# Kernel tuning notes

Hardware: AMD Instinct MI355X
Metric: run time of the kernel (lower is better)

Reference implementation:

```python
import jax, jax.numpy as jnp
import numpy as np

B, S, H, L, C = 32, 512, 768, 512, 3  # batch, seq, hidden, max_length, num_classes


def _lin_init(k, fan_in, shape):
    return jax.random.normal(k, shape, jnp.float32) * (1.0 / np.sqrt(fan_in))


def setup_inputs() -> dict:
    key = jax.random.key(0)
    ks = jax.random.split(key, 18)
    return {
        "tokens": jax.random.normal(ks[0], (B, S, H), jnp.float32),
        # shared Q/K/V projections (used for both token- and feature-attention)
        "Wq": _lin_init(ks[1], H, (H, H)), "bq": jnp.zeros((H,), jnp.float32),
        "Wk": _lin_init(ks[2], H, (H, H)), "bk": jnp.zeros((H,), jnp.float32),
        "Wv": _lin_init(ks[3], H, (H, H)), "bv": jnp.zeros((H,), jnp.float32),
        # TSGSA: Linear(H,1)+ReLU gate over tokens
        "W_ts": _lin_init(ks[4], H, (H, 1)), "b_ts": jnp.zeros((1,), jnp.float32),
        # FSGSA: Linear(max_length,1)+ReLU gate over padded seq axis (also reused for FGSA per source bug)
        "W_fs": _lin_init(ks[5], L, (L, 1)), "b_fs": jnp.zeros((1,), jnp.float32),
        # TGSA: Linear(H,H)+Sigmoid gate
        "W_tg": _lin_init(ks[6], H, (H, H)), "b_tg": jnp.zeros((H,), jnp.float32),
        # fnn: Linear(7H,H) -> Linear(H,C)
        "W1": _lin_init(ks[7], 7 * H, (7 * H, H)), "b1": jnp.zeros((H,), jnp.float32),
        "W2": _lin_init(ks[8], H, (H, C)), "b2": jnp.zeros((C,), jnp.float32),
    }


def _ln(x):
    # LayerNorm over (seq, hidden) jointly, eps=1e-8; freshly-instantiated affine params are identity
    m = jnp.mean(x, axis=(1, 2), keepdims=True)
    v = jnp.var(x, axis=(1, 2), keepdims=True)
    return (x - m) * jax.lax.rsqrt(v + 1e-8)


def reference(tokens, Wq, bq, Wk, bk, Wv, bv, W_ts, b_ts, W_fs, b_fs, W_tg, b_tg, W1, b1, W2, b2):
    scale = 1.0 / np.sqrt(H)
    Q = tokens @ Wq + bq  # [B,S,H]
    K = tokens @ Wk + bk
    V = tokens @ Wv + bv
    # token-direction self-attention: softmax(Q K^T / sqrt(H)) V
    att = jax.nn.softmax(jnp.einsum('bsh,bth->bst', Q, K) * scale, axis=-1)  # [B,S,S]
    TSA = jnp.einsum('bst,bth->bsh', att, V)
    # feature-direction self-attention: V @ softmax(Q^T K / sqrt(H))
    attN = jax.nn.softmax(jnp.einsum('bsh,bsg->bhg', Q, K) * scale, axis=-1)  # [B,H,H]
    FSA = jnp.einsum('bsh,bhg->bsg', V, attN)
    # gate branches
    TSGSA = jax.nn.relu(tokens @ W_ts + b_ts) * tokens  # [B,S,1]*[B,S,H]
    tpad = jnp.pad(tokens.transpose(0, 2, 1), ((0, 0), (0, 0), (0, L - S)))  # [B,H,L]
    gate_f = jax.nn.relu(tpad @ W_fs + b_fs)  # [B,H,1]
    FSGSA = (gate_f * tokens.transpose(0, 2, 1)).transpose(0, 2, 1)  # [B,S,H]
    TGSA = jax.nn.sigmoid(tokens @ W_tg + b_tg) * tokens
    FGSA = FSGSA  # source bug: FGSA branch applies self.FSGSA, identical to FSGSA
    out_all = jnp.concatenate(
        [tokens, _ln(TSA), _ln(FSA), _ln(TGSA), _ln(FGSA), _ln(TSGSA), _ln(FSGSA)], axis=2)  # [B,S,7H]
    pooled = jnp.mean(out_all, axis=1)  # [B,7H]
    return (pooled @ W1 + b1) @ W2 + b2  # [B,C]
```

## Files before the change

kernel.cpp:

```cpp
#include <hip/hip_runtime.h>
#include <cmath>

typedef unsigned short u16;
typedef __attribute__((ext_vector_type(4))) float f32x4;
typedef __attribute__((ext_vector_type(4))) unsigned int u32x4;
typedef __attribute__((ext_vector_type(8))) __bf16 bf16x8;

__device__ __forceinline__ u16 f2b(float f) {
  unsigned int u = __builtin_bit_cast(unsigned int, f);
  return (u16)((u + 0x7fffu + ((u >> 16) & 1u)) >> 16);
}
__device__ __forceinline__ float b2f(u16 h) {
  unsigned int u = ((unsigned int)h) << 16;
  return __builtin_bit_cast(float, u);
}

__device__ __forceinline__ void glds16(const u16* g, u16* l) {
  __builtin_amdgcn_global_load_lds(
      (const __attribute__((address_space(1))) void*)g,
      (__attribute__((address_space(3))) void*)l, 16, 0, 0);
}

template <int EPI>
__global__ __launch_bounds__(256) void gemm_f_k(
    const u16* __restrict__ Ap, const u16* __restrict__ Bp, u16* __restrict__ Cp,
    u16* __restrict__ CpT, const float* __restrict__ bias,
    const float* __restrict__ tokp, float* __restrict__ colsum,
    float* __restrict__ bstat, int K, int lda, int ldb, int ldc, long sA,
    long sB, long sC, float scale) {
  __shared__ alignas(16) u16 smem[4][4096];

  const int gx = gridDim.x, gxy = gx * gridDim.y;
  const int nwg = gxy * gridDim.z;
  int orig = (blockIdx.z * gridDim.y + blockIdx.y) * gx + blockIdx.x;
  int gwi = (orig & 7) * (nwg >> 3) + (orig >> 3);
  const int z = gwi / gxy;
  int rem = gwi - z * gxy;
  const int ty = rem / gx, tx = rem - ty * gx;
  const int tileM = ty << 7, tileN = tx << 7;

  const u16* Abase = Ap + (size_t)z * sA;
  const u16* Bbase = Bp + (size_t)z * sB;

  const int tid = threadIdx.x;
  const int lane = tid & 63, w = tid >> 6;
  const int wr = (w >> 1) << 6, wc = (w & 1) << 6;
  const int fr = lane & 15, fg = lane >> 4;

  f32x4 acc[4][4];
#pragma unroll
  for (int i = 0; i < 4; ++i)
#pragma unroll
    for (int j = 0; j < 4; ++j) acc[i][j] = (f32x4){0.f, 0.f, 0.f, 0.f};

  const int srow = (w << 5) + (lane >> 2);
  const int scol = (((lane & 3) ^ ((lane >> 3) & 3)) << 3);
  const u16* gA = Abase + (size_t)(tileM + srow) * lda + scol;
  const u16* gB = Bbase + (size_t)(tileN + srow) * ldb + scol;
  const int ldsw = (w << 5) * 32;

  auto STAGE = [&](int buf, int k0) {
    const u16* ga = gA + k0;
    const u16* gb = gB + k0;
    u16* la = &smem[buf * 2][ldsw];
    u16* lb = &smem[buf * 2 + 1][ldsw];
    glds16(ga, la);
    glds16(ga + (size_t)16 * lda, la + 512);
    glds16(gb, lb);
    glds16(gb + (size_t)16 * ldb, lb + 512);
  };

  const int col_off = ((fg ^ ((fr >> 1) & 3)) << 3);

  const int nt = K >> 5;
  STAGE(0, 0);
  int cur = 0;
  for (int t = 0; t < nt; ++t) {
    if (t + 1 < nt) {
      STAGE(cur ^ 1, (t + 1) << 5);
      asm volatile("s_waitcnt vmcnt(4)" ::: "memory");
    } else {
      asm volatile("s_waitcnt vmcnt(0)" ::: "memory");
    }
    __builtin_amdgcn_s_barrier();
    asm volatile("" ::: "memory");
    const u16* Ab = smem[cur * 2];
    const u16* Bb = smem[cur * 2 + 1];
    bf16x8 av[4], bw[4];
#pragma unroll
    for (int m = 0; m < 4; ++m)
      av[m] = *(const bf16x8*)&Ab[(wr + (m << 4) + fr) * 32 + col_off];
#pragma unroll
    for (int n = 0; n < 4; ++n)
      bw[n] = *(const bf16x8*)&Bb[(wc + (n << 4) + fr) * 32 + col_off];
#pragma unroll
    for (int m = 0; m < 4; ++m)
#pragma unroll
      for (int n = 0; n < 4; ++n)
        acc[m][n] =
            __builtin_amdgcn_mfma_f32_16x16x32_bf16(av[m], bw[n], acc[m][n], 0, 0, 0);
    asm volatile("" ::: "memory");
    __builtin_amdgcn_s_barrier();
    cur ^= 1;
  }

  if constexpr (EPI == 0 || EPI == 2) {
    int cbuf = 0, nbase = tileN;
    if constexpr (EPI == 0) { cbuf = tileN / 768; nbase = tileN - cbuf * 768; }
    u16* Cz = Cp + (EPI == 0 ? (size_t)cbuf * sC : (size_t)z * sC);
#pragma unroll
    for (int m = 0; m < 4; ++m) {
#pragma unroll
      for (int n = 0; n < 4; ++n) {
        const int gcol = tileN + wc + (n << 4) + fr;
        const int lcol = nbase + wc + (n << 4) + fr;
#pragma unroll
        for (int r = 0; r < 4; ++r) {
          const int grow = tileM + wr + (m << 4) + (fg << 2) + r;
          float v = acc[m][n][r];
          if constexpr (EPI == 0) v += bias[gcol];
          else v *= scale;
          Cz[(size_t)grow * ldc + lcol] = f2b(v);
        }
      }
    }
    if constexpr (EPI == 0) {
      u16* Ct = CpT + (size_t)cbuf * sC;
#pragma unroll
      for (int m = 0; m < 4; ++m) {
#pragma unroll
        for (int n = 0; n < 4; ++n) {
          const int gcol = tileN + wc + (n << 4) + fr;
          const int lcol = nbase + wc + (n << 4) + fr;
          const int grow0 = tileM + wr + (m << 4) + (fg << 2);
          union { u16 u[4]; unsigned long long q; } pk;
#pragma unroll
          for (int r = 0; r < 4; ++r) pk.u[r] = f2b(acc[m][n][r] + bias[gcol]);
          *(unsigned long long*)&Ct[(size_t)lcol * 16384 + grow0] = pk.q;
        }
      }
    }
  } else {
    __shared__ float scol_s[128];
    __shared__ float sred[2];
    if (tid < 128) scol_s[tid] = 0.f;
    if (tid == 0) { sred[0] = 0.f; sred[1] = 0.f; }
    __syncthreads();
    float ls = 0.f, lq = 0.f;
#pragma unroll
    for (int n = 0; n < 4; ++n) {
      float cpart = 0.f;
      const int gcol = tileN + wc + (n << 4) + fr;
#pragma unroll
      for (int m = 0; m < 4; ++m) {
#pragma unroll
        for (int r = 0; r < 4; ++r) {
          float v = acc[m][n][r];
          if constexpr (EPI == 1) {
            const int grow = tileM + wr + (m << 4) + (fg << 2) + r;
            float pre = v + bias[gcol];
            float g = 1.f / (1.f + __expf(-pre));
            v = g * tokp[(size_t)grow * 768 + gcol];
          }
          cpart += v; ls += v; lq += v * v;
        }
      }
      atomicAdd(&scol_s[wc + (n << 4) + fr], cpart);
    }
    atomicAdd(&sred[0], ls);
    atomicAdd(&sred[1], lq);
    __syncthreads();
    const int b = (EPI == 1) ? (tileM >> 9) : z;
    if (tid < 128) atomicAdd(&colsum[(size_t)b * 768 + tileN + tid], scol_s[tid]);
    if (tid == 0) {
      atomicAdd(&bstat[b], sred[0]);
      atomicAdd(&bstat[32 + b], sred[1]);
    }
  }
}

__global__ __launch_bounds__(256) void cvt_tok_k(const float* __restrict__ in,
                                                 u16* __restrict__ out) {
  const size_t i = ((size_t)blockIdx.x * 256 + threadIdx.x) * 8;
  f32x4 a = *(const f32x4*)(in + i), b = *(const f32x4*)(in + i + 4);
  union { u16 u[8]; u32x4 q; } pk;
#pragma unroll
  for (int j = 0; j < 4; ++j) { pk.u[j] = f2b(a[j]); pk.u[4 + j] = f2b(b[j]); }
  *(u32x4*)(out + i) = pk.q;
}

__global__ __launch_bounds__(256) void transpose_w_k(const float* __restrict__ W,
                                                     u16* __restrict__ WT) {
  __shared__ float t[64][65];
  const int r0 = blockIdx.y << 6, c0 = blockIdx.x << 6;
  for (int i = threadIdx.x; i < 4096; i += 256) {
    int r = i >> 6, c = i & 63;
    t[r][c] = W[(size_t)(r0 + r) * 768 + c0 + c];
  }
  __syncthreads();
  for (int i = threadIdx.x; i < 4096; i += 256) {
    int rr = i >> 6, cc = i & 63;
    WT[(size_t)(c0 + rr) * 768 + r0 + cc] = f2b(t[cc][rr]);
  }
}

__global__ __launch_bounds__(256) void transpose_bf_k(const u16* __restrict__ in,
                                                      u16* __restrict__ out) {
  __shared__ u16 t[64][72];
  const size_t base = (size_t)blockIdx.z * 589824;
  const int r0 = blockIdx.y << 6, c0 = blockIdx.x << 6;
  for (int i = threadIdx.x; i < 512; i += 256) {
    int r = i >> 3, c8 = (i & 7) << 3;
    union { u32x4 q; u16 u[8]; } pk;
    pk.q = *(const u32x4*)&in[base + (size_t)(r0 + r) * 768 + c0 + c8];
#pragma unroll
    for (int j = 0; j < 8; ++j) t[c8 + j][r] = pk.u[j];
  }
  __syncthreads();
  for (int i = threadIdx.x; i < 512; i += 256) {
    int r = i >> 3, c8 = (i & 7) << 3;
    *(u32x4*)&out[base + (size_t)(c0 + r) * 768 + r0 + c8] = *(u32x4*)&t[r][c8];
  }
}

template <int LEN>
__global__ __launch_bounds__(256) void softmax_k(u16* __restrict__ data) {
  constexpr int NP = LEN / 256;
  const int row = blockIdx.x, tid = threadIdx.x;
  u16* p = data + (size_t)row * LEN;
  const int lane = tid & 63, wid = tid >> 6;
  float v[NP];
  float mx = -1e30f;
#pragma unroll
  for (int i = 0; i < NP; ++i) { v[i] = b2f(p[tid + (i << 8)]); mx = fmaxf(mx, v[i]); }
#pragma unroll
  for (int o = 32; o > 0; o >>= 1) mx = fmaxf(mx, __shfl_xor(mx, o));
  __shared__ float red[4], red2[4];
  if (lane == 0) red[wid] = mx;
  __syncthreads();
  mx = fmaxf(fmaxf(red[0], red[1]), fmaxf(red[2], red[3]));
  float sum = 0.f;
#pragma unroll
  for (int i = 0; i < NP; ++i) { v[i] = __expf(v[i] - mx); sum += v[i]; }
#pragma unroll
  for (int o = 32; o > 0; o >>= 1) sum += __shfl_xor(sum, o);
  if (lane == 0) red2[wid] = sum;
  __syncthreads();
  sum = red2[0] + red2[1] + red2[2] + red2[3];
  const float inv = 1.f / sum;
#pragma unroll
  for (int i = 0; i < NP; ++i) p[tid + (i << 8)] = f2b(v[i] * inv);
}

__global__ __launch_bounds__(256) void row_stats_k(
    const float* __restrict__ tok, const float* __restrict__ Wts,
    const float* __restrict__ bts, float* __restrict__ gate_t,
    float* __restrict__ rowsum, float* __restrict__ rowsumsq) {
  const int wid = threadIdx.x >> 6, lane = threadIdx.x & 63;
  const int row = blockIdx.x * 4 + wid;
  const float* p = tok + (size_t)row * 768;
  float s = 0.f, q = 0.f, g = 0.f;
#pragma unroll
  for (int i = 0; i < 12; ++i) {
    float t = p[lane + i * 64];
    s += t; q += t * t; g += t * Wts[lane + i * 64];
  }
#pragma unroll
  for (int o = 32; o > 0; o >>= 1) {
    s += __shfl_xor(s, o); q += __shfl_xor(q, o); g += __shfl_xor(g, o);
  }
  if (lane == 0) {
    gate_t[row] = fmaxf(g + bts[0], 0.f);
    rowsum[row] = s;
    rowsumsq[row] = q;
  }
}

__global__ __launch_bounds__(256) void col_stats_k(
    const float* __restrict__ tok, const float* __restrict__ Wfs,
    const float* __restrict__ bfs, const float* __restrict__ gate_t,
    float* __restrict__ gate_f, float* __restrict__ colsum_tok,
    float* __restrict__ colsumsq_tok, float* __restrict__ colsum_tsg) {
  const int b = blockIdx.x, h = blockIdx.y * 256 + threadIdx.x;
  const float* p = tok + (size_t)b * 512 * 768 + h;
  const float* gt = gate_t + b * 512;
  float cs = 0.f, cq = 0.f, gf = 0.f, tg = 0.f;
#pragma unroll 4
  for (int s = 0; s < 512; ++s) {
    float t = p[(size_t)s * 768];
    cs += t; cq += t * t; gf += t * Wfs[s]; tg += t * gt[s];
  }
  const int idx = b * 768 + h;
  gate_f[idx] = fmaxf(gf + bfs[0], 0.f);
  colsum_tok[idx] = cs;
  colsumsq_tok[idx] = cq;
  colsum_tsg[idx] = tg;
}

__global__ __launch_bounds__(256) void batch_stats_k(
    const float* __restrict__ gate_t, const float* __restrict__ rowsum,
    const float* __restrict__ rowsumsq, const float* __restrict__ gate_f,
    const float* __restrict__ colsum_tok, const float* __restrict__ colsumsq_tok,
    float* __restrict__ st) {
  __shared__ float red[4][256];
  const int b = blockIdx.x, tid = threadIdx.x;
  float ts = 0.f, tq = 0.f, fs = 0.f, fq = 0.f;
  for (int s = tid; s < 512; s += 256) {
    float g = gate_t[b * 512 + s];
    ts += g * rowsum[b * 512 + s];
    tq += g * g * rowsumsq[b * 512 + s];
  }
  for (int h = tid; h < 768; h += 256) {
    float g = gate_f[b * 768 + h];
    fs += g * colsum_tok[b * 768 + h];
    fq += g * g * colsumsq_tok[b * 768 + h];
  }
  red[0][tid] = ts; red[1][tid] = tq; red[2][tid] = fs; red[3][tid] = fq;
  __syncthreads();
  for (int o = 128; o > 0; o >>= 1) {
    if (tid < o) {
      red[0][tid] += red[0][tid + o];
      red[1][tid] += red[1][tid + o];
      red[2][tid] += red[2][tid + o];
      red[3][tid] += red[3][tid + o];
    }
    __syncthreads();
  }
  if (tid == 0) {
    st[b] = red[0][0]; st[32 + b] = red[1][0];
    st[64 + b] = red[2][0]; st[96 + b] = red[3][0];
  }
}

__global__ __launch_bounds__(768) void pooled_k(
    const float* __restrict__ colsum_tok, const float* __restrict__ colsum_tsa,
    const float* __restrict__ bstat_tsa, const float* __restrict__ colsum_fsa,
    const float* __restrict__ bstat_fsa, const float* __restrict__ colsum_tgsa,
    const float* __restrict__ bstat_tgsa, const float* __restrict__ colsum_tsg,
    const float* __restrict__ gate_f, const float* __restrict__ st,
    float* __restrict__ pooled) {
  const int b = blockIdx.x, h = threadIdx.x;
  const float invS = 1.f / 512.f, invN = 1.f / (512.f * 768.f);
  const int i = b * 768 + h;
  float* pr = pooled + (size_t)b * 5376;
  pr[h] = colsum_tok[i] * invS;
  auto lnslot = [&](int slot, float cs, float bs, float bq) {
    float m = bs * invN;
    float var = bq * invN - m * m;
    pr[slot * 768 + h] = (cs * invS - m) * rsqrtf(var + 1e-8f);
  };
  lnslot(1, colsum_tsa[i], bstat_tsa[b], bstat_tsa[32 + b]);
  lnslot(2, colsum_fsa[i], bstat_fsa[b], bstat_fsa[32 + b]);
  lnslot(3, colsum_tgsa[i], bstat_tgsa[b], bstat_tgsa[32 + b]);
  const float fsg_cs = gate_f[i] * colsum_tok[i];
  lnslot(4, fsg_cs, st[64 + b], st[96 + b]);
  lnslot(5, colsum_tsg[i], st[b], st[32 + b]);
  lnslot(6, fsg_cs, st[64 + b], st[96 + b]);
}

__global__ __launch_bounds__(256) void fnn1_k(const float* __restrict__ pooled,
                                              const float* __restrict__ W1,
                                              float* __restrict__ tmp1) {
  __shared__ float sp[128][36];
  const int c0 = blockIdx.x << 7, k0 = blockIdx.y << 7;
  const int tid = threadIdx.x;
  for (int i = tid; i < 4096; i += 256) {
    int b = i >> 7, j = i & 127;
    sp[j][b] = pooled[(size_t)b * 5376 + k0 + j];
  }
  __syncthreads();
  const int c = c0 + (tid & 127);
  const int u = (tid >> 7) << 4;
  float acc[16];
#pragma unroll
  for (int t = 0; t < 16; ++t) acc[t] = 0.f;
#pragma unroll 4
  for (int j = 0; j < 128; ++j) {
    float w = W1[(size_t)(k0 + j) * 768 + c];
    const f32x4* row = (const f32x4*)&sp[j][u];
#pragma unroll
    for (int t4 = 0; t4 < 4; ++t4) {
      f32x4 v = row[t4];
#pragma unroll
      for (int r = 0; r < 4; ++r) acc[t4 * 4 + r] += v[r] * w;
    }
  }
#pragma unroll
  for (int t = 0; t < 16; ++t) atomicAdd(&tmp1[(u + t) * 768 + c], acc[t]);
}

__global__ __launch_bounds__(256) void fnn2_k(const float* __restrict__ tmp1,
                                              const float* __restrict__ b1,
                                              const float* __restrict__ W2,
                                              const float* __restrict__ b2,
                                              float* __restrict__ out) {
  const int gw = blockIdx.x * 4 + (threadIdx.x >> 6);
  const int lane = threadIdx.x & 63;
  const int b = gw / 3, c = gw % 3;
  float a = 0.f;
#pragma unroll
  for (int i = 0; i < 12; ++i) {
    int k = lane + i * 64;
    a += (tmp1[b * 768 + k] + b1[k]) * W2[k * 3 + c];
  }
#pragma unroll
  for (int o = 32; o > 0; o >>= 1) a += __shfl_xor(a, o);
  if (lane == 0) out[b * 3 + c] = a + b2[c];
}

extern "C" void kernel_launch(void* const* d_in, const int* in_sizes, int n_in,
                              void* d_out, int out_size, void* d_ws, size_t ws_size,
                              hipStream_t stream) {
  const float* tokens = (const float*)d_in[0];
  const float* Wq = (const float*)d_in[1];
  const float* bq = (const float*)d_in[2];
  const float* Wk = (const float*)d_in[3];
  const float* bk = (const float*)d_in[4];
  const float* Wv = (const float*)d_in[5];
  const float* bv = (const float*)d_in[6];
  const float* Wts = (const float*)d_in[7];
  const float* bts = (const float*)d_in[8];
  const float* Wfs = (const float*)d_in[9];
  const float* bfs = (const float*)d_in[10];
  const float* Wtg = (const float*)d_in[11];
  const float* btg = (const float*)d_in[12];
  const float* W1 = (const float*)d_in[13];
  const float* b1 = (const float*)d_in[14];
  const float* W2 = (const float*)d_in[15];
  const float* b2 = (const float*)d_in[16];
  float* out = (float*)d_out;

  char* ws = (char*)d_ws;
  size_t off = 0;
  auto take = [&](size_t bytes) -> char* {
    char* p = ws + off;
    off += (bytes + 255) & ~(size_t)255;
    return p;
  };
  u16* tokb = (u16*)take((size_t)16384 * 768 * 2);
  u16* WqT = (u16*)take((size_t)768 * 768 * 2);
  u16* WkT = (u16*)take((size_t)768 * 768 * 2);
  u16* WvT = (u16*)take((size_t)768 * 768 * 2);
  u16* WtgT = (u16*)take((size_t)768 * 768 * 2);
  u16* Qb = (u16*)take((size_t)16384 * 768 * 2);
  u16* Kb = (u16*)take((size_t)16384 * 768 * 2);
  u16* Vb = (u16*)take((size_t)16384 * 768 * 2);
  u16* Qt = (u16*)take((size_t)768 * 16384 * 2);
  u16* Kt = (u16*)take((size_t)768 * 16384 * 2);
  u16* Vt = (u16*)take((size_t)768 * 16384 * 2);
  u16* attb = (u16*)take((size_t)32 * 512 * 512 * 2);
  u16* attNb = (u16*)take((size_t)32 * 768 * 768 * 2);
  u16* attNt = Qt;
  float* bias3 = (float*)take(2304 * 4);
  char* zbase = ws + off;
  float* colsum_tsa = (float*)take(24576 * 4);
  float* colsum_fsa = (float*)take(24576 * 4);
  float* colsum_tgsa = (float*)take(24576 * 4);
  float* bstat_tsa = (float*)take(64 * 4);
  float* bstat_fsa = (float*)take(64 * 4);
  float* bstat_tgsa = (float*)take(64 * 4);
  float* tmp1 = (float*)take((size_t)32 * 768 * 4);
  size_t zbytes = (size_t)((ws + off) - zbase);
  float* colsum_tsg = (float*)take(24576 * 4);
  float* gate_t = (float*)take(16384 * 4);
  float* rowsum = (float*)take(16384 * 4);
  float* rowsumsq = (float*)take(16384 * 4);
  float* gate_f = (float*)take(24576 * 4);
  float* colsum_tok = (float*)take(24576 * 4);
  float* colsumsq_tok = (float*)take(24576 * 4);
  float* st4 = (float*)take(128 * 4);
  float* pooled = (float*)take((size_t)32 * 5376 * 4);

  hipMemsetAsync(zbase, 0, zbytes, stream);
  hipMemcpyAsync(bias3, bq, 768 * 4, hipMemcpyDeviceToDevice, stream);
  hipMemcpyAsync(bias3 + 768, bk, 768 * 4, hipMemcpyDeviceToDevice, stream);
  hipMemcpyAsync(bias3 + 1536, bv, 768 * 4, hipMemcpyDeviceToDevice, stream);

  const float scale = 1.0f / sqrtf(768.0f);
  const dim3 blk(256);

  cvt_tok_k<<<6144, blk, 0, stream>>>(tokens, tokb);
  transpose_w_k<<<dim3(12, 12), blk, 0, stream>>>(Wq, WqT);
  transpose_w_k<<<dim3(12, 12), blk, 0, stream>>>(Wk, WkT);
  transpose_w_k<<<dim3(12, 12), blk, 0, stream>>>(Wv, WvT);
  transpose_w_k<<<dim3(12, 12), blk, 0, stream>>>(Wtg, WtgT);

  gemm_f_k<0><<<dim3(18, 128, 1), blk, 0, stream>>>(
      tokb, WqT, Qb, Qt, bias3, nullptr, nullptr, nullptr, 768, 768, 768, 768,
      0, 0, 12582912, 0.f);
  gemm_f_k<1><<<dim3(6, 128, 1), blk, 0, stream>>>(
      tokb, WtgT, nullptr, nullptr, btg, tokens, colsum_tgsa, bstat_tgsa, 768,
      768, 768, 0, 0, 0, 0, 0.f);

  gemm_f_k<2><<<dim3(6, 6, 32), blk, 0, stream>>>(
      Qt, Kt, attNb, nullptr, nullptr, nullptr, nullptr, nullptr, 512, 16384,
      16384, 768, 512, 512, 589824, scale);
  softmax_k<768><<<24576, 256, 0, stream>>>(attNb);
  transpose_bf_k<<<dim3(12, 12, 32), blk, 0, stream>>>(attNb, attNt);

  gemm_f_k<2><<<dim3(4, 4, 32), blk, 0, stream>>>(
      Qb, Kb, attb, nullptr, nullptr, nullptr, nullptr, nullptr, 768, 768, 768,
      512, 393216, 393216, 262144, scale);
  softmax_k<512><<<16384, 256, 0, stream>>>(attb);

  gemm_f_k<3><<<dim3(6, 4, 32), blk, 0, stream>>>(
      attb, Vt, nullptr, nullptr, nullptr, nullptr, colsum_tsa, bstat_tsa, 512,
      512, 16384, 0, 262144, 512, 0, 0.f);
  gemm_f_k<3><<<dim3(6, 4, 32), blk, 0, stream>>>(
      Vb, attNt, nullptr, nullptr, nullptr, nullptr, colsum_fsa, bstat_fsa, 768,
      768, 768, 0, 393216, 589824, 0, 0.f);

  row_stats_k<<<4096, blk, 0, stream>>>(tokens, Wts, bts, gate_t, rowsum, rowsumsq);
  col_stats_k<<<dim3(32, 3), blk, 0, stream>>>(tokens, Wfs, bfs, gate_t, gate_f,
                                               colsum_tok, colsumsq_tok, colsum_tsg);
  batch_stats_k<<<32, blk, 0, stream>>>(gate_t, rowsum, rowsumsq, gate_f,
                                        colsum_tok, colsumsq_tok, st4);

  pooled_k<<<32, 768, 0, stream>>>(colsum_tok, colsum_tsa, bstat_tsa, colsum_fsa,
                                   bstat_fsa, colsum_tgsa, bstat_tgsa, colsum_tsg,
                                   gate_f, st4, pooled);
  fnn1_k<<<dim3(6, 42), blk, 0, stream>>>(pooled, W1, tmp1);
  fnn2_k<<<24, blk, 0, stream>>>(tmp1, b1, W2, b2, out);
}
```

Measured before the change: 464.3 us.

## Fuse gate GEMM into QKV GEMM, compute attN transposed, stage transposes in LDS

```diff
diff --git a/kernel.cpp b/kernel.cpp
--- a/kernel.cpp
+++ b/kernel.cpp
@@ -25,10 +25,12 @@
 __global__ __launch_bounds__(256) void gemm_f_k(
     const u16* __restrict__ Ap, const u16* __restrict__ Bp, u16* __restrict__ Cp,
     u16* __restrict__ CpT, const float* __restrict__ bias,
-    const float* __restrict__ tokp, float* __restrict__ colsum,
+    const u16* __restrict__ tokp, float* __restrict__ colsum,
     float* __restrict__ bstat, int K, int lda, int ldb, int ldc, long sA,
     long sB, long sC, float scale) {
   __shared__ alignas(16) u16 smem[4][4096];
+  __shared__ float scol_s[128];
+  __shared__ float sred[2];
 
   const int gx = gridDim.x, gxy = gx * gridDim.y;
   const int nwg = gxy * gridDim.z;
@@ -104,45 +106,100 @@
     cur ^= 1;
   }
 
-  if constexpr (EPI == 0 || EPI == 2) {
-    int cbuf = 0, nbase = tileN;
-    if constexpr (EPI == 0) { cbuf = tileN / 768; nbase = tileN - cbuf * 768; }
-    u16* Cz = Cp + (EPI == 0 ? (size_t)cbuf * sC : (size_t)z * sC);
-#pragma unroll
-    for (int m = 0; m < 4; ++m) {
-#pragma unroll
-      for (int n = 0; n < 4; ++n) {
-        const int gcol = tileN + wc + (n << 4) + fr;
-        const int lcol = nbase + wc + (n << 4) + fr;
-#pragma unroll
-        for (int r = 0; r < 4; ++r) {
-          const int grow = tileM + wr + (m << 4) + (fg << 2) + r;
-          float v = acc[m][n][r];
-          if constexpr (EPI == 0) v += bias[gcol];
-          else v *= scale;
-          Cz[(size_t)grow * ldc + lcol] = f2b(v);
-        }
-      }
-    }
-    if constexpr (EPI == 0) {
-      u16* Ct = CpT + (size_t)cbuf * sC;
+  if constexpr (EPI == 0) {
+    const int cbuf = tileN / 768;
+    const int nbase = tileN - cbuf * 768;
+    if (cbuf < 3) {
+      u16* Cz = Cp + (size_t)cbuf * sC;
 #pragma unroll
       for (int m = 0; m < 4; ++m) {
 #pragma unroll
         for (int n = 0; n < 4; ++n) {
           const int gcol = tileN + wc + (n << 4) + fr;
           const int lcol = nbase + wc + (n << 4) + fr;
-          const int grow0 = tileM + wr + (m << 4) + (fg << 2);
+          const float bv2 = bias[gcol];
+#pragma unroll
+          for (int r = 0; r < 4; ++r) {
+            const int grow = tileM + wr + (m << 4) + (fg << 2) + r;
+            Cz[(size_t)grow * 768 + lcol] = f2b(acc[m][n][r] + bv2);
+          }
+        }
+      }
+      u16* tr = &smem[0][0];
+      const int xr = fr << 3;
+#pragma unroll
+      for (int m = 0; m < 4; ++m) {
+#pragma unroll
+        for (int n = 0; n < 4; ++n) {
+          const int gcol = tileN + wc + (n << 4) + fr;
+          const float bv2 = bias[gcol];
           union { u16 u[4]; unsigned long long q; } pk;
 #pragma unroll
-          for (int r = 0; r < 4; ++r) pk.u[r] = f2b(acc[m][n][r] + bias[gcol]);
-          *(unsigned long long*)&Ct[(size_t)lcol * 16384 + grow0] = pk.q;
+          for (int r = 0; r < 4; ++r) pk.u[r] = f2b(acc[m][n][r] + bv2);
+          const int rowb = wr + (m << 4) + (fg << 2);
+          *(unsigned long long*)&tr[(wc + (n << 4) + fr) * 128 + (rowb ^ xr)] =
+              pk.q;
         }
       }
+      __syncthreads();
+      u16* Ct = CpT + (size_t)cbuf * sC;
+      const int col = tid >> 1, rh = (tid & 1) << 6;
+      const int xc = (col & 15) << 3;
+      const u16* trc = &tr[col * 128];
+      u16* outc = &Ct[(size_t)(nbase + col) * 16384 + tileM];
+#pragma unroll
+      for (int i = 0; i < 8; ++i) {
+        const int r0 = rh + (i << 3);
+        *(u32x4*)&outc[r0] = *(const u32x4*)&trc[r0 ^ xc];
+      }
+    } else {
+      if (tid < 128) scol_s[tid] = 0.f;
+      if (tid == 0) { sred[0] = 0.f; sred[1] = 0.f; }
+      __syncthreads();
+      float ls = 0.f, lq = 0.f;
+#pragma unroll
+      for (int n = 0; n < 4; ++n) {
+        float cpart = 0.f;
+        const int gcol = tileN + wc + (n << 4) + fr;
+        const int lcol = nbase + wc + (n << 4) + fr;
+        const float bv2 = bias[gcol];
+#pragma unroll
+        for (int m = 0; m < 4; ++m) {
+#pragma unroll
+          for (int r = 0; r < 4; ++r) {
+            const int grow = tileM + wr + (m << 4) + (fg << 2) + r;
+            float g = 1.f / (1.f + __expf(-(acc[m][n][r] + bv2)));
+            float v = g * b2f(tokp[(size_t)grow * 768 + lcol]);
+            cpart += v; ls += v; lq += v * v;
+          }
+        }
+        atomicAdd(&scol_s[wc + (n << 4) + fr], cpart);
+      }
+      atomicAdd(&sred[0], ls);
+      atomicAdd(&sred[1], lq);
+      __syncthreads();
+      const int b = tileM >> 9;
+      if (tid < 128) atomicAdd(&colsum[(size_t)b * 768 + nbase + tid], scol_s[tid]);
+      if (tid == 0) {
+        atomicAdd(&bstat[b], sred[0]);
+        atomicAdd(&bstat[32 + b], sred[1]);
+      }
+    }
+  } else if constexpr (EPI == 2) {
+    u16* Cz = Cp + (size_t)z * sC;
+#pragma unroll
+    for (int m = 0; m < 4; ++m) {
+#pragma unroll
+      for (int n = 0; n < 4; ++n) {
+        const int gcol = tileN + wc + (n << 4) + fr;
+#pragma unroll
+        for (int r = 0; r < 4; ++r) {
+          const int grow = tileM + wr + (m << 4) + (fg << 2) + r;
+          Cz[(size_t)grow * ldc + gcol] = f2b(acc[m][n][r] * scale);
+        }
+      }
     }
   } else {
-    __shared__ float scol_s[128];
-    __shared__ float sred[2];
     if (tid < 128) scol_s[tid] = 0.f;
     if (tid == 0) { sred[0] = 0.f; sred[1] = 0.f; }
     __syncthreads();
@@ -150,18 +207,11 @@
 #pragma unroll
     for (int n = 0; n < 4; ++n) {
       float cpart = 0.f;
-      const int gcol = tileN + wc + (n << 4) + fr;
 #pragma unroll
       for (int m = 0; m < 4; ++m) {
 #pragma unroll
         for (int r = 0; r < 4; ++r) {
           float v = acc[m][n][r];
-          if constexpr (EPI == 1) {
-            const int grow = tileM + wr + (m << 4) + (fg << 2) + r;
-            float pre = v + bias[gcol];
-            float g = 1.f / (1.f + __expf(-pre));
-            v = g * tokp[(size_t)grow * 768 + gcol];
-          }
           cpart += v; ls += v; lq += v * v;
         }
       }
@@ -170,23 +220,46 @@
     atomicAdd(&sred[0], ls);
     atomicAdd(&sred[1], lq);
     __syncthreads();
-    const int b = (EPI == 1) ? (tileM >> 9) : z;
-    if (tid < 128) atomicAdd(&colsum[(size_t)b * 768 + tileN + tid], scol_s[tid]);
+    if (tid < 128) atomicAdd(&colsum[(size_t)z * 768 + tileN + tid], scol_s[tid]);
     if (tid == 0) {
-      atomicAdd(&bstat[b], sred[0]);
-      atomicAdd(&bstat[32 + b], sred[1]);
-    }
-  }
-}
-
-__global__ __launch_bounds__(256) void cvt_tok_k(const float* __restrict__ in,
-                                                 u16* __restrict__ out) {
-  const size_t i = ((size_t)blockIdx.x * 256 + threadIdx.x) * 8;
-  f32x4 a = *(const f32x4*)(in + i), b = *(const f32x4*)(in + i + 4);
-  union { u16 u[8]; u32x4 q; } pk;
-#pragma unroll
-  for (int j = 0; j < 4; ++j) { pk.u[j] = f2b(a[j]); pk.u[4 + j] = f2b(b[j]); }
-  *(u32x4*)(out + i) = pk.q;
+      atomicAdd(&bstat[z], sred[0]);
+      atomicAdd(&bstat[32 + z], sred[1]);
+    }
+  }
+}
+
+__global__ __launch_bounds__(256) void cvt_row_k(
+    const float* __restrict__ tok, u16* __restrict__ tokb,
+    const float* __restrict__ Wts, const float* __restrict__ bts,
+    float* __restrict__ gate_t, float* __restrict__ rowsum,
+    float* __restrict__ rowsumsq) {
+  const int w = threadIdx.x >> 6, lane = threadIdx.x & 63;
+  const int row = blockIdx.x * 4 + w;
+  const float* p = tok + (size_t)row * 768;
+  u16* q = tokb + (size_t)row * 768;
+  float s = 0.f, sq = 0.f, g = 0.f;
+#pragma unroll
+  for (int i = 0; i < 3; ++i) {
+    const int idx = (i * 64 + lane) << 2;
+    f32x4 v = *(const f32x4*)(p + idx);
+    f32x4 wv = *(const f32x4*)(Wts + idx);
+    union { u16 u[4]; unsigned long long q8; } pk;
+#pragma unroll
+    for (int j = 0; j < 4; ++j) {
+      s += v[j]; sq += v[j] * v[j]; g += v[j] * wv[j];
+      pk.u[j] = f2b(v[j]);
+    }
+    *(unsigned long long*)(q + idx) = pk.q8;
+  }
+#pragma unroll
+  for (int o = 32; o > 0; o >>= 1) {
+    s += __shfl_xor(s, o); sq += __shfl_xor(sq, o); g += __shfl_xor(g, o);
+  }
+  if (lane == 0) {
+    gate_t[row] = fmaxf(g + bts[0], 0.f);
+    rowsum[row] = s;
+    rowsumsq[row] = sq;
+  }
 }
 
 __global__ __launch_bounds__(256) void transpose_w_k(const float* __restrict__ W,
@@ -201,25 +274,6 @@
   for (int i = threadIdx.x; i < 4096; i += 256) {
     int rr = i >> 6, cc = i & 63;
     WT[(size_t)(c0 + rr) * 768 + r0 + cc] = f2b(t[cc][rr]);
-  }
-}
-
-__global__ __launch_bounds__(256) void transpose_bf_k(const u16* __restrict__ in,
-                                                      u16* __restrict__ out) {
-  __shared__ u16 t[64][72];
-  const size_t base = (size_t)blockIdx.z * 589824;
-  const int r0 = blockIdx.y << 6, c0 = blockIdx.x << 6;
-  for (int i = threadIdx.x; i < 512; i += 256) {
-    int r = i >> 3, c8 = (i & 7) << 3;
-    union { u32x4 q; u16 u[8]; } pk;
-    pk.q = *(const u32x4*)&in[base + (size_t)(r0 + r) * 768 + c0 + c8];
-#pragma unroll
-    for (int j = 0; j < 8; ++j) t[c8 + j][r] = pk.u[j];
-  }
-  __syncthreads();
-  for (int i = threadIdx.x; i < 512; i += 256) {
-    int r = i >> 3, c8 = (i & 7) << 3;
-    *(u32x4*)&out[base + (size_t)(c0 + r) * 768 + r0 + c8] = *(u32x4*)&t[r][c8];
   }
 }
 
@@ -252,42 +306,38 @@
   for (int i = 0; i < NP; ++i) p[tid + (i << 8)] = f2b(v[i] * inv);
 }
 
-__global__ __launch_bounds__(256) void row_stats_k(
-    const float* __restrict__ tok, const float* __restrict__ Wts,
-    const float* __restrict__ bts, float* __restrict__ gate_t,
-    float* __restrict__ rowsum, float* __restrict__ rowsumsq) {
-  const int wid = threadIdx.x >> 6, lane = threadIdx.x & 63;
-  const int row = blockIdx.x * 4 + wid;
-  const float* p = tok + (size_t)row * 768;
-  float s = 0.f, q = 0.f, g = 0.f;
-#pragma unroll
-  for (int i = 0; i < 12; ++i) {
-    float t = p[lane + i * 64];
-    s += t; q += t * t; g += t * Wts[lane + i * 64];
-  }
-#pragma unroll
-  for (int o = 32; o > 0; o >>= 1) {
-    s += __shfl_xor(s, o); q += __shfl_xor(q, o); g += __shfl_xor(g, o);
-  }
-  if (lane == 0) {
-    gate_t[row] = fmaxf(g + bts[0], 0.f);
-    rowsum[row] = s;
-    rowsumsq[row] = q;
+__global__ __launch_bounds__(64) void colsoftmax_k(u16* __restrict__ data) {
+  const int b = blockIdx.x;
+  const int h = blockIdx.y * 64 + threadIdx.x;
+  u16* p = data + (size_t)b * 589824 + h;
+  float m = -1e30f, s = 0.f;
+#pragma unroll 4
+  for (int g = 0; g < 768; ++g) {
+    float v = b2f(p[(size_t)g * 768]);
+    float mn = fmaxf(m, v);
+    s = s * __expf(m - mn) + __expf(v - mn);
+    m = mn;
+  }
+  const float inv = 1.f / s;
+#pragma unroll 4
+  for (int g = 0; g < 768; ++g) {
+    float v = b2f(p[(size_t)g * 768]);
+    p[(size_t)g * 768] = f2b(__expf(v - m) * inv);
   }
 }
 
 __global__ __launch_bounds__(256) void col_stats_k(
-    const float* __restrict__ tok, const float* __restrict__ Wfs,
+    const u16* __restrict__ tokb, const float* __restrict__ Wfs,
     const float* __restrict__ bfs, const float* __restrict__ gate_t,
     float* __restrict__ gate_f, float* __restrict__ colsum_tok,
     float* __restrict__ colsumsq_tok, float* __restrict__ colsum_tsg) {
   const int b = blockIdx.x, h = blockIdx.y * 256 + threadIdx.x;
-  const float* p = tok + (size_t)b * 512 * 768 + h;
+  const u16* p = tokb + (size_t)b * 512 * 768 + h;
   const float* gt = gate_t + b * 512;
   float cs = 0.f, cq = 0.f, gf = 0.f, tg = 0.f;
 #pragma unroll 4
   for (int s = 0; s < 512; ++s) {
-    float t = p[(size_t)s * 768];
+    float t = b2f(p[(size_t)s * 768]);
     cs += t; cq += t * t; gf += t * Wfs[s]; tg += t * gt[s];
   }
   const int idx = b * 768 + h;
@@ -449,9 +499,8 @@
   u16* Kt = (u16*)take((size_t)768 * 16384 * 2);
   u16* Vt = (u16*)take((size_t)768 * 16384 * 2);
   u16* attb = (u16*)take((size_t)32 * 512 * 512 * 2);
-  u16* attNb = (u16*)take((size_t)32 * 768 * 768 * 2);
-  u16* attNt = Qt;
-  float* bias3 = (float*)take(2304 * 4);
+  u16* attNt = (u16*)take((size_t)32 * 768 * 768 * 2);
+  float* bias4 = (float*)take(3072 * 4);
   char* zbase = ws + off;
   float* colsum_tsa = (float*)take(24576 * 4);
   float* colsum_fsa = (float*)take(24576 * 4);
@@ -472,31 +521,29 @@
   float* pooled = (float*)take((size_t)32 * 5376 * 4);
 
   hipMemsetAsync(zbase, 0, zbytes, stream);
-  hipMemcpyAsync(bias3, bq, 768 * 4, hipMemcpyDeviceToDevice, stream);
-  hipMemcpyAsync(bias3 + 768, bk, 768 * 4, hipMemcpyDeviceToDevice, stream);
-  hipMemcpyAsync(bias3 + 1536, bv, 768 * 4, hipMemcpyDeviceToDevice, stream);
+  hipMemcpyAsync(bias4, bq, 768 * 4, hipMemcpyDeviceToDevice, stream);
+  hipMemcpyAsync(bias4 + 768, bk, 768 * 4, hipMemcpyDeviceToDevice, stream);
+  hipMemcpyAsync(bias4 + 1536, bv, 768 * 4, hipMemcpyDeviceToDevice, stream);
+  hipMemcpyAsync(bias4 + 2304, btg, 768 * 4, hipMemcpyDeviceToDevice, stream);
 
   const float scale = 1.0f / sqrtf(768.0f);
   const dim3 blk(256);
 
-  cvt_tok_k<<<6144, blk, 0, stream>>>(tokens, tokb);
+  cvt_row_k<<<4096, blk, 0, stream>>>(tokens, tokb, Wts, bts, gate_t, rowsum,
+                                      rowsumsq);
   transpose_w_k<<<dim3(12, 12), blk, 0, stream>>>(Wq, WqT);
   transpose_w_k<<<dim3(12, 12), blk, 0, stream>>>(Wk, WkT);
   transpose_w_k<<<dim3(12, 12), blk, 0, stream>>>(Wv, WvT);
   transpose_w_k<<<dim3(12, 12), blk, 0, stream>>>(Wtg, WtgT);
 
-  gemm_f_k<0><<<dim3(18, 128, 1), blk, 0, stream>>>(
-      tokb, WqT, Qb, Qt, bias3, nullptr, nullptr, nullptr, 768, 768, 768, 768,
-      0, 0, 12582912, 0.f);
-  gemm_f_k<1><<<dim3(6, 128, 1), blk, 0, stream>>>(
-      tokb, WtgT, nullptr, nullptr, btg, tokens, colsum_tgsa, bstat_tgsa, 768,
-      768, 768, 0, 0, 0, 0, 0.f);
+  gemm_f_k<0><<<dim3(24, 128, 1), blk, 0, stream>>>(
+      tokb, WqT, Qb, Qt, bias4, tokb, colsum_tgsa, bstat_tgsa, 768, 768, 768,
+      768, 0, 0, 12582912, 0.f);
 
   gemm_f_k<2><<<dim3(6, 6, 32), blk, 0, stream>>>(
-      Qt, Kt, attNb, nullptr, nullptr, nullptr, nullptr, nullptr, 512, 16384,
+      Kt, Qt, attNt, nullptr, nullptr, nullptr, nullptr, nullptr, 512, 16384,
       16384, 768, 512, 512, 589824, scale);
-  softmax_k<768><<<24576, 256, 0, stream>>>(attNb);
-  transpose_bf_k<<<dim3(12, 12, 32), blk, 0, stream>>>(attNb, attNt);
+  colsoftmax_k<<<dim3(32, 12), 64, 0, stream>>>(attNt);
 
   gemm_f_k<2><<<dim3(4, 4, 32), blk, 0, stream>>>(
       Qb, Kb, attb, nullptr, nullptr, nullptr, nullptr, nullptr, 768, 768, 768,
@@ -510,8 +557,7 @@
       Vb, attNt, nullptr, nullptr, nullptr, nullptr, colsum_fsa, bstat_fsa, 768,
       768, 768, 0, 393216, 589824, 0, 0.f);
 
-  row_stats_k<<<4096, blk, 0, stream>>>(tokens, Wts, bts, gate_t, rowsum, rowsumsq);
-  col_stats_k<<<dim3(32, 3), blk, 0, stream>>>(tokens, Wfs, bfs, gate_t, gate_f,
+  col_stats_k<<<dim3(32, 3), blk, 0, stream>>>(tokb, Wfs, bfs, gate_t, gate_f,
                                                colsum_tok, colsumsq_tok, colsum_tsg);
   batch_stats_k<<<32, blk, 0, stream>>>(gate_t, rowsum, rowsumsq, gate_f,
                                         colsum_tok, colsumsq_tok, st4);
```

Result: slower. 644.2 us (+38.8%).
